# Performance work log

Measured on AMD Instinct MI355X. Metric: run time of the kernel, lower is better.

## Reference

```python
import jax, jax.numpy as jnp
import numpy as np

B, S, T = 16, 128, 128
E, H, D = 512, 512, 1024      # emb, encoder hidden, decoder hidden
VIN, VOUT = 10000, 10000


def setup_inputs() -> dict:
    key = jax.random.key(0)
    ks = iter(jax.random.split(key, 32))
    def w(shape, s=0.02):
        return jax.random.normal(next(ks), shape, jnp.float32) * s
    return {
        "x": jax.random.randint(next(ks), (B, S), 0, VIN),
        "gs_output": jax.random.randint(next(ks), (B, T), 0, VOUT),
        "in_emb": w((VIN, E)),
        "out_emb": w((VOUT, E)),
        "enc_wih0": w((2, 4 * H, E)), "enc_whh0": w((2, 4 * H, H)), "enc_b0": w((2, 4 * H)),
        "enc_wih1": w((2, 4 * H, 2 * H)), "enc_whh1": w((2, 4 * H, H)), "enc_b1": w((2, 4 * H)),
        "dec_wih0": w((4 * D, 2 * H + E)), "dec_whh0": w((4 * D, D)), "dec_b0": w((4 * D,)),
        "dec_wih1": w((4 * D, D)), "dec_whh1": w((4 * D, D)), "dec_b1": w((4 * D,)),
        "attn_w": w((D, 2 * H + D)), "attn_b": w((D,)),
        "attn_v": jax.random.uniform(next(ks), (D,), jnp.float32),
        "out_w": w((VOUT, D)), "out_b": w((VOUT,)),
    }


def _lstm_cell(x, h, c, wih, whh, b):
    # PyTorch gate order: i, f, g, o
    g = x @ wih.T + h @ whh.T + b
    i, f, gg, o = jnp.split(g, 4, axis=-1)
    c = jax.nn.sigmoid(f) * c + jax.nn.sigmoid(i) * jnp.tanh(gg)
    h = jax.nn.sigmoid(o) * jnp.tanh(c)
    return h, c


def _lstm_scan(xs, wih, whh, b, reverse=False):
    # xs: [T, B, in] time-major; returns hidden states [T, B, H]
    Bn, Hh = xs.shape[1], whh.shape[1]
    z = jnp.zeros((Bn, Hh), xs.dtype)
    def step(carry, x):
        h, c = _lstm_cell(x, carry[0], carry[1], wih, whh, b)
        return (h, c), h
    _, hs = jax.lax.scan(step, (z, z), xs, reverse=reverse)
    return hs


def reference(x, gs_output, in_emb, out_emb,
              enc_wih0, enc_whh0, enc_b0, enc_wih1, enc_whh1, enc_b1,
              dec_wih0, dec_whh0, dec_b0, dec_wih1, dec_whh1, dec_b1,
              attn_w, attn_b, attn_v, out_w, out_b):
    # padding_idx=0 rows are zero (matches nn.Embedding(padding_idx=0))
    in_emb = in_emb.at[0].set(0.0)
    out_emb = out_emb.at[0].set(0.0)
    Bn, Sn = x.shape

    # ---- bidirectional 2-layer encoder (eval mode, dropout off) ----
    xs = in_emb[x].transpose(1, 0, 2)  # [S, B, E]
    l0 = jnp.concatenate([
        _lstm_scan(xs, enc_wih0[0], enc_whh0[0], enc_b0[0]),
        _lstm_scan(xs, enc_wih0[1], enc_whh0[1], enc_b0[1], reverse=True)], -1)
    enc = jnp.concatenate([
        _lstm_scan(l0, enc_wih1[0], enc_whh1[0], enc_b1[0]),
        _lstm_scan(l0, enc_wih1[1], enc_whh1[1], enc_b1[1], reverse=True)], -1)
    enc_out = enc.transpose(1, 0, 2)  # [B, S, 2H]

    dec_layers = ((dec_wih0, dec_whh0, dec_b0), (dec_wih1, dec_whh1, dec_b1))

    def dec_step(h, c, inp):
        hs, cs = [], []
        for l, (wih, whh, b) in enumerate(dec_layers):
            nh, nc = _lstm_cell(inp, h[l], c[l], wih, whh, b)
            hs.append(nh); cs.append(nc); inp = nh
        return jnp.stack(hs), jnp.stack(cs), inp

    # torch primes decoder_hidden with one zero-input step from zero state
    h = jnp.zeros((2, Bn, D), jnp.float32)
    c = jnp.zeros((2, Bn, D), jnp.float32)
    h, c, _ = dec_step(h, c, jnp.zeros((Bn, 2 * H + E), jnp.float32))

    gs_emb = out_emb[gs_output].transpose(1, 0, 2)  # [T, B, E]

    def step(carry, emb_t):
        h, c, last_emb = carry
        q = c[-1]  # torch uses decoder_hidden[-1][-1] = last-layer CELL state
        qrep = jnp.broadcast_to(q[:, None, :], (Bn, Sn, D))
        energy = jnp.tanh(jnp.einsum('bsk,dk->bsd', jnp.concatenate([qrep, enc_out], -1), attn_w) + attn_b)
        a = jax.nn.softmax(energy @ attn_v, axis=1)           # [B, S]
        weighted = jnp.einsum('bs,bsh->bh', a, enc_out)       # [B, 2H]
        h2, c2, top = dec_step(h, c, jnp.concatenate([weighted, last_emb], -1))
        logits = top @ out_w.T + out_b                        # [B, Vout]
        return (h2, c2, emb_t), logits

    init = (h, c, jnp.zeros((Bn, E), jnp.float32))
    _, outs = jax.lax.scan(step, init, gs_emb)                # [T, B, Vout]
    return outs.transpose(1, 0, 2)                            # [B, T, Vout]
```

## Files before the change

### kernel.cpp

```cpp
#include <hip/hip_runtime.h>

#define BB 16
#define SS 128
#define TT 128
#define EE 512
#define HH 512
#define DD 1024
#define VO 10000

#define FMA4(A, W, X)              \
  A = fmaf((W).x, (X).x, A);       \
  A = fmaf((W).y, (X).y, A);       \
  A = fmaf((W).z, (X).z, A);       \
  A = fmaf((W).w, (X).w, A)

__device__ __forceinline__ float wred(float s) {
#pragma unroll
  for (int off = 32; off >= 1; off >>= 1) s += __shfl_xor(s, off, 64);
  return s;
}
__device__ __forceinline__ float sigm(float x) { return 1.f / (1.f + expf(-x)); }

__device__ __forceinline__ void stv(float* p, float v) {
  __hip_atomic_store(p, v, __ATOMIC_RELAXED, __HIP_MEMORY_SCOPE_AGENT);
}

__device__ __forceinline__ void gbar2(unsigned* bar, int lb, int nblk, unsigned target) {
  asm volatile("s_waitcnt vmcnt(0) lgkmcnt(0)" ::: "memory");
  __syncthreads();
  if (threadIdx.x == 0)
    __hip_atomic_store(bar + lb * 16, target, __ATOMIC_RELAXED, __HIP_MEMORY_SCOPE_AGENT);
  if (lb == 0) {
    for (int i = threadIdx.x; i < nblk; i += blockDim.x)
      while (__hip_atomic_load(bar + i * 16, __ATOMIC_RELAXED, __HIP_MEMORY_SCOPE_AGENT) <
             target)
        __builtin_amdgcn_s_sleep(1);
    __syncthreads();
    if (threadIdx.x == 0)
      __hip_atomic_store(bar + 8192, target, __ATOMIC_RELAXED, __HIP_MEMORY_SCOPE_AGENT);
  }
  if (threadIdx.x == 0)
    while (__hip_atomic_load(bar + 8192, __ATOMIC_RELAXED, __HIP_MEMORY_SCOPE_AGENT) <
           target)
      __builtin_amdgcn_s_sleep(1);
  __syncthreads();
}

__global__ void gather_k(const int* __restrict__ idx, const float* __restrict__ emb,
                         float* __restrict__ out, int Sn) {
  const int s = blockIdx.x, b = blockIdx.y, tid = threadIdx.x;
  const int id = idx[b * Sn + s];
  float4 v = make_float4(0.f, 0.f, 0.f, 0.f);
  if (id != 0) v = ((const float4*)(emb + (size_t)id * EE))[tid];
  ((float4*)(out + ((size_t)s * BB + b) * EE))[tid] = v;
}

template <int K>
__global__ void gemv16b_k(const float* __restrict__ X, int ldx,
                          const float* __restrict__ W, int ldw,
                          float* __restrict__ G, int M, size_t wz, size_t gz) {
  const int lane = threadIdx.x & 63;
  const int n = blockIdx.x * 4 + (threadIdx.x >> 6);
  const int mg = blockIdx.y;
  const int z = blockIdx.z;
  const float* Xr = X + (size_t)mg * 16 * ldx;
  const float* Wn = W + (size_t)z * wz + (size_t)n * ldw;
  float acc[16];
#pragma unroll
  for (int j = 0; j < 16; ++j) acc[j] = 0.f;
#pragma unroll
  for (int it = 0; it < K / 256; ++it) {
    const int k = it * 256 + lane * 4;
    const float4 w4 = *(const float4*)&Wn[k];
#pragma unroll
    for (int j = 0; j < 16; ++j) {
      const float4 xv = *(const float4*)&Xr[(size_t)j * ldx + k];
      FMA4(acc[j], w4, xv);
    }
  }
#pragma unroll
  for (int j = 0; j < 16; ++j) acc[j] = wred(acc[j]);
  float sel = 0.f;
#pragma unroll
  for (int j = 0; j < 16; ++j)
    if (lane == j) sel = acc[j];
  if (lane < 16) G[(size_t)z * gz + (size_t)n * M + mg * 16 + lane] = sel;
}

__global__ __launch_bounds__(512, 4) void enc_mega7_k(
    const float* __restrict__ gx, const float* __restrict__ whh,
    const float* __restrict__ bias, float* __restrict__ h_all,
    float* __restrict__ seq, int seq_ts, int seq_bs, unsigned* __restrict__ barbase) {
  const int tid = threadIdx.x, lane = tid & 63, lw = tid >> 6;
  const int dir = blockIdx.x >> 7;
  const int lb = blockIdx.x & 127;
  const int w2 = lb * 8 + lw;
  const int d = w2 >> 1, bq = w2 & 1;
  unsigned* bar = barbase + dir * 16384;

  __shared__ float hs[16][512];

  float wr[4][8];
  const float* wsrc = whh + (size_t)dir * (4 * HH * HH);
#pragma unroll
  for (int g = 0; g < 4; ++g)
#pragma unroll
    for (int j = 0; j < 8; ++j)
      wr[g][j] = wsrc[(size_t)(g * HH + d) * HH + j * 64 + lane];
  float bv[4];
#pragma unroll
  for (int g = 0; g < 4; ++g) bv[g] = bias[dir * 4 * HH + g * HH + d];
  const float* gxz = gx + (size_t)dir * ((size_t)4 * HH * 2048);
  float creg = 0.f;
  unsigned bt = 0;

  for (int t = 0; t < SS; ++t) {
    const int idx = dir ? (SS - 1 - t) : t;
    const float* hp = h_all + ((size_t)t * 2 + dir) * (BB * HH);
    for (int i = tid; i < BB * HH / 4; i += 512)
      *(float4*)&((float*)hs)[i * 4] = *(const float4*)&hp[i * 4];
    __syncthreads();
    float acc[4][8];
#pragma unroll
    for (int g = 0; g < 4; ++g)
#pragma unroll
      for (int j = 0; j < 8; ++j) acc[g][j] = 0.f;
#pragma unroll
    for (int kb = 0; kb < 8; ++kb) {
      const int k = kb * 64 + lane;
#pragma unroll
      for (int j = 0; j < 8; ++j) {
        const float xv = hs[bq * 8 + j][k];
#pragma unroll
        for (int g = 0; g < 4; ++g) acc[g][j] = fmaf(wr[g][kb], xv, acc[g][j]);
      }
    }
#pragma unroll
    for (int g = 0; g < 4; ++g)
#pragma unroll
      for (int j = 0; j < 8; ++j) acc[g][j] = wred(acc[g][j]);
    float s0 = 0.f, s1 = 0.f, s2 = 0.f, s3 = 0.f;
#pragma unroll
    for (int j = 0; j < 8; ++j)
      if (lane == j) { s0 = acc[0][j]; s1 = acc[1][j]; s2 = acc[2][j]; s3 = acc[3][j]; }
    if (lane < 8) {
      const int b = bq * 8 + lane;
      const int m = idx * 16 + b;
      const float gi = sigm(s0 + bv[0] + gxz[(size_t)(0 * HH + d) * 2048 + m]);
      const float gf = sigm(s1 + bv[1] + gxz[(size_t)(1 * HH + d) * 2048 + m]);
      const float gg = tanhf(s2 + bv[2] + gxz[(size_t)(2 * HH + d) * 2048 + m]);
      const float go = sigm(s3 + bv[3] + gxz[(size_t)(3 * HH + d) * 2048 + m]);
      const float cn = gf * creg + gi * gg;
      creg = cn;
      const float hv = go * tanhf(cn);
      stv(h_all + ((size_t)(t + 1) * 2 + dir) * (BB * HH) + b * HH + d, hv);
      seq[(size_t)idx * seq_ts + (size_t)b * seq_bs + dir * HH + d] = hv;
    }
    gbar2(bar, lb, 128, ++bt);
  }
}

__global__ __launch_bounds__(1024, 4) void dec_mega7_k(
    const float* __restrict__ gs_emb, const float* __restrict__ encWe,
    const float* __restrict__ enc_out, const float* __restrict__ attn_w,
    const float* __restrict__ attn_b, const float* __restrict__ attn_v,
    const float* __restrict__ wih0, const float* __restrict__ whh0,
    const float* __restrict__ b0, const float* __restrict__ wih1,
    const float* __restrict__ whh1, const float* __restrict__ b1,
    const float* __restrict__ zeros, float* __restrict__ h0_all,
    float* __restrict__ h1_all, float* __restrict__ c1_all, float* __restrict__ wtd_all,
    float* __restrict__ qW_all, float* __restrict__ scores_all,
    unsigned* __restrict__ bar) {
  const int tid = threadIdx.x, lane = tid & 63, lw = tid >> 6;
  const int blk = blockIdx.x;
  const int w = blk * 16 + lw;
  const int d = w >> 2, bq = w & 3;
  const int b_att = blk >> 4, shard = blk & 15;

  __shared__ float sco[SS];
  __shared__ float sred[16][64];

  const float* w0i0 = wih0 + (size_t)(0 * DD + d) * 1536;
  const float* w0i1 = wih0 + (size_t)(1 * DD + d) * 1536;
  const float* w0i2 = wih0 + (size_t)(2 * DD + d) * 1536;
  const float* w0i3 = wih0 + (size_t)(3 * DD + d) * 1536;
  const float* w0h0 = whh0 + (size_t)(0 * DD + d) * 1024;
  const float* w0h1 = whh0 + (size_t)(1 * DD + d) * 1024;
  const float* w0h2 = whh0 + (size_t)(2 * DD + d) * 1024;
  const float* w0h3 = whh0 + (size_t)(3 * DD + d) * 1024;
  const float* w1i0 = wih1 + (size_t)(0 * DD + d) * 1024;
  const float* w1i1 = wih1 + (size_t)(1 * DD + d) * 1024;
  const float* w1i2 = wih1 + (size_t)(2 * DD + d) * 1024;
  const float* w1i3 = wih1 + (size_t)(3 * DD + d) * 1024;
  const float* w1h0 = whh1 + (size_t)(0 * DD + d) * 1024;
  const float* w1h1 = whh1 + (size_t)(1 * DD + d) * 1024;
  const float* w1h2 = whh1 + (size_t)(2 * DD + d) * 1024;
  const float* w1h3 = whh1 + (size_t)(3 * DD + d) * 1024;
  float bv0[4], bv1[4];
#pragma unroll
  for (int g = 0; g < 4; ++g) { bv0[g] = b0[g * DD + d]; bv1[g] = b1[g * DD + d]; }
  const float abv = attn_b[d];
  float c0 = 0.f, c1 = 0.f;
  unsigned bt = 0;

  if (lane < 4) {
    const float cn = sigm(bv0[0]) * tanhf(bv0[2]);
    c0 = cn;
    stv(h0_all + (bq * 4 + lane) * DD + d, sigm(bv0[3]) * tanhf(cn));
  }
  gbar2(bar, blk, 256, ++bt);
  {
    float acc[4][4];
#pragma unroll
    for (int g = 0; g < 4; ++g)
#pragma unroll
      for (int j = 0; j < 4; ++j) acc[g][j] = 0.f;
#pragma unroll
    for (int it = 0; it < 4; ++it) {
      const int k = it * 256 + lane * 4;
      const float4 q0 = *(const float4*)&w1i0[k];
      const float4 q1 = *(const float4*)&w1i1[k];
      const float4 q2 = *(const float4*)&w1i2[k];
      const float4 q3 = *(const float4*)&w1i3[k];
#pragma unroll
      for (int j = 0; j < 4; ++j) {
        const float4 xv = *(const float4*)&h0_all[(bq * 4 + j) * DD + k];
        FMA4(acc[0][j], q0, xv);
        FMA4(acc[1][j], q1, xv);
        FMA4(acc[2][j], q2, xv);
        FMA4(acc[3][j], q3, xv);
      }
    }
#pragma unroll
    for (int g = 0; g < 4; ++g)
#pragma unroll
      for (int j = 0; j < 4; ++j) acc[g][j] = wred(acc[g][j]);
    float s[4] = {0.f, 0.f, 0.f, 0.f};
#pragma unroll
    for (int j = 0; j < 4; ++j)
      if (lane == j) { s[0] = acc[0][j]; s[1] = acc[1][j]; s[2] = acc[2][j]; s[3] = acc[3][j]; }
    if (lane < 4) {
      const int b = bq * 4 + lane;
      const float cn = sigm(s[0] + bv1[0]) * tanhf(s[2] + bv1[2]);
      c1 = cn;
      stv(c1_all + b * DD + d, cn);
      stv(h1_all + b * DD + d, sigm(s[3] + bv1[3]) * tanhf(cn));
    }
  }
  gbar2(bar, blk, 256, ++bt);

  for (int t = 0; t < TT; ++t) {
    {
      const float* cb = c1_all + (size_t)t * (BB * DD);
      const float* wq = attn_w + (size_t)d * 2048;
      float qa[4] = {0.f, 0.f, 0.f, 0.f};
#pragma unroll
      for (int it = 0; it < 4; ++it) {
        const int k = it * 256 + lane * 4;
        const float4 w4 = *(const float4*)&wq[k];
#pragma unroll
        for (int j = 0; j < 4; ++j) {
          const float4 xv = *(const float4*)&cb[(bq * 4 + j) * DD + k];
          FMA4(qa[j], w4, xv);
        }
      }
#pragma unroll
      for (int j = 0; j < 4; ++j) qa[j] = wred(qa[j]);
      float sel = 0.f;
#pragma unroll
      for (int j = 0; j < 4; ++j)
        if (lane == j) sel = qa[j];
      if (lane < 4)
        stv(qW_all + (size_t)t * (BB * DD) + (bq * 4 + lane) * DD + d, sel + abv);
    }
    gbar2(bar, blk, 256, ++bt);
    if (lw < 8) {
      const int s = shard * 8 + lw;
      const float* ew = encWe + ((size_t)(b_att * SS + s)) * DD;
      const float* qb = qW_all + (size_t)t * (BB * DD) + b_att * DD;
      float a = 0.f;
#pragma unroll
      for (int it = 0; it < 4; ++it) {
        const int k = it * 256 + lane * 4;
        const float4 e4 = *(const float4*)&ew[k];
        const float4 q4 = *(const float4*)&qb[k];
        const float4 v4 = *(const float4*)&attn_v[k];
        a += v4.x * tanhf(q4.x + e4.x) + v4.y * tanhf(q4.y + e4.y) +
             v4.z * tanhf(q4.z + e4.z) + v4.w * tanhf(q4.w + e4.w);
      }
      a = wred(a);
      if (lane == 0) stv(scores_all + (size_t)t * (BB * SS) + b_att * SS + s, a);
    }
    gbar2(bar, blk, 256, ++bt);
    {
      if (tid < SS) sco[tid] = scores_all[(size_t)t * (BB * SS) + b_att * SS + tid];
      __syncthreads();
      float m = -1e30f;
      for (int s = 0; s < SS; ++s) m = fmaxf(m, sco[s]);
      __syncthreads();
      if (tid < SS) sco[tid] = expf(sco[tid] - m);
      __syncthreads();
      float sum = 0.f;
      for (int s = 0; s < SS; ++s) sum += sco[s];
      const float inv = 1.f / sum;
      float p = 0.f;
#pragma unroll
      for (int i = 0; i < 8; ++i) {
        const int s = lw * 8 + i;
        p += sco[s] * enc_out[((size_t)(b_att * SS + s)) * DD + shard * 64 + lane];
      }
      sred[lw][lane] = p;
      __syncthreads();
      if (lw == 0) {
        float a2 = 0.f;
#pragma unroll
        for (int i = 0; i < 16; ++i) a2 += sred[i][lane];
        stv(wtd_all + (size_t)t * (BB * DD) + b_att * DD + shard * 64 + lane, a2 * inv);
      }
    }
    gbar2(bar, blk, 256, ++bt);
    {
      const float* xw = wtd_all + (size_t)t * (BB * DD);
      const float* em = t ? gs_emb + (size_t)(t - 1) * (BB * EE) : zeros;
      const float* hp = h0_all + (size_t)t * (BB * DD);
      float acc[4][4];
#pragma unroll
      for (int g = 0; g < 4; ++g)
#pragma unroll
        for (int j = 0; j < 4; ++j) acc[g][j] = 0.f;
#pragma unroll
      for (int it = 0; it < 4; ++it) {
        const int k = it * 256 + lane * 4;
        const float4 q0 = *(const float4*)&w0i0[k];
        const float4 q1 = *(const float4*)&w0i1[k];
        const float4 q2 = *(const float4*)&w0i2[k];
        const float4 q3 = *(const float4*)&w0i3[k];
#pragma unroll
        for (int j = 0; j < 4; ++j) {
          const float4 xv = *(const float4*)&xw[(bq * 4 + j) * DD + k];
          FMA4(acc[0][j], q0, xv);
          FMA4(acc[1][j], q1, xv);
          FMA4(acc[2][j], q2, xv);
          FMA4(acc[3][j], q3, xv);
        }
      }
#pragma unroll
      for (int it = 4; it < 6; ++it) {
        const int k = it * 256 + lane * 4;
        const float4 q0 = *(const float4*)&w0i0[k];
        const float4 q1 = *(const float4*)&w0i1[k];
        const float4 q2 = *(const float4*)&w0i2[k];
        const float4 q3 = *(const float4*)&w0i3[k];
#pragma unroll
        for (int j = 0; j < 4; ++j) {
          const float4 xv = *(const float4*)&em[(bq * 4 + j) * EE + (k - 1024)];
          FMA4(acc[0][j], q0, xv);
          FMA4(acc[1][j], q1, xv);
          FMA4(acc[2][j], q2, xv);
          FMA4(acc[3][j], q3, xv);
        }
      }
#pragma unroll
      for (int it = 0; it < 4; ++it) {
        const int k = it * 256 + lane * 4;
        const float4 q0 = *(const float4*)&w0h0[k];
        const float4 q1 = *(const float4*)&w0h1[k];
        const float4 q2 = *(const float4*)&w0h2[k];
        const float4 q3 = *(const float4*)&w0h3[k];
#pragma unroll
        for (int j = 0; j < 4; ++j) {
          const float4 xv = *(const float4*)&hp[(bq * 4 + j) * DD + k];
          FMA4(acc[0][j], q0, xv);
          FMA4(acc[1][j], q1, xv);
          FMA4(acc[2][j], q2, xv);
          FMA4(acc[3][j], q3, xv);
        }
      }
#pragma unroll
      for (int g = 0; g < 4; ++g)
#pragma unroll
        for (int j = 0; j < 4; ++j) acc[g][j] = wred(acc[g][j]);
      float s[4] = {0.f, 0.f, 0.f, 0.f};
#pragma unroll
      for (int j = 0; j < 4; ++j)
        if (lane == j) { s[0] = acc[0][j]; s[1] = acc[1][j]; s[2] = acc[2][j]; s[3] = acc[3][j]; }
      if (lane < 4) {
        const int b = bq * 4 + lane;
        const float cn = sigm(s[1] + bv0[1]) * c0 + sigm(s[0] + bv0[0]) * tanhf(s[2] + bv0[2]);
        c0 = cn;
        stv(h0_all + (size_t)(t + 1) * (BB * DD) + b * DD + d,
            sigm(s[3] + bv0[3]) * tanhf(cn));
      }
    }
    gbar2(bar, blk, 256, ++bt);
    {
      const float* h0 = h0_all + (size_t)(t + 1) * (BB * DD);
      const float* h1p = h1_all + (size_t)t * (BB * DD);
      float acc[4][4];
#pragma unroll
      for (int g = 0; g < 4; ++g)
#pragma unroll
        for (int j = 0; j < 4; ++j) acc[g][j] = 0.f;
#pragma unroll
      for (int it = 0; it < 4; ++it) {
        const int k = it * 256 + lane * 4;
        const float4 q0 = *(const float4*)&w1i0[k];
        const float4 q1 = *(const float4*)&w1i1[k];
        const float4 q2 = *(const float4*)&w1i2[k];
        const float4 q3 = *(const float4*)&w1i3[k];
#pragma unroll
        for (int j = 0; j < 4; ++j) {
          const float4 xv = *(const float4*)&h0[(bq * 4 + j) * DD + k];
          FMA4(acc[0][j], q0, xv);
          FMA4(acc[1][j], q1, xv);
          FMA4(acc[2][j], q2, xv);
          FMA4(acc[3][j], q3, xv);
        }
      }
#pragma unroll
      for (int it = 0; it < 4; ++it) {
        const int k = it * 256 + lane * 4;
        const float4 q0 = *(const float4*)&w1h0[k];
        const float4 q1 = *(const float4*)&w1h1[k];
        const float4 q2 = *(const float4*)&w1h2[k];
        const float4 q3 = *(const float4*)&w1h3[k];
#pragma unroll
        for (int j = 0; j < 4; ++j) {
          const float4 xv = *(const float4*)&h1p[(bq * 4 + j) * DD + k];
          FMA4(acc[0][j], q0, xv);
          FMA4(acc[1][j], q1, xv);
          FMA4(acc[2][j], q2, xv);
          FMA4(acc[3][j], q3, xv);
        }
      }
#pragma unroll
      for (int g = 0; g < 4; ++g)
#pragma unroll
        for (int j = 0; j < 4; ++j) acc[g][j] = wred(acc[g][j]);
      float s[4] = {0.f, 0.f, 0.f, 0.f};
#pragma unroll
      for (int j = 0; j < 4; ++j)
        if (lane == j) { s[0] = acc[0][j]; s[1] = acc[1][j]; s[2] = acc[2][j]; s[3] = acc[3][j]; }
      if (lane < 4) {
        const int b = bq * 4 + lane;
        const float cn = sigm(s[1] + bv1[1]) * c1 + sigm(s[0] + bv1[0]) * tanhf(s[2] + bv1[2]);
        c1 = cn;
        stv(c1_all + (size_t)(t + 1) * (BB * DD) + b * DD + d, cn);
        stv(h1_all + (size_t)(t + 1) * (BB * DD) + b * DD + d,
            sigm(s[3] + bv1[3]) * tanhf(cn));
      }
    }
    gbar2(bar, blk, 256, ++bt);
  }
}

__global__ __launch_bounds__(512) void encwe2_k(const float* __restrict__ enc_out,
                                                const float* __restrict__ attn_w,
                                                float* __restrict__ encWe) {
  const int tid = threadIdx.x, lane = tid & 63, lw = tid >> 6;
  const int mg = blockIdx.x;
  const int nq = blockIdx.y;
  __shared__ float xsl[16][1024];
  for (int i = tid; i < 16 * 1024 / 4; i += 512)
    *(float4*)&((float*)xsl)[i * 4] =
        *(const float4*)&enc_out[(size_t)mg * 16 * 1024 + i * 4];
  __syncthreads();
#pragma unroll 1
  for (int nn = 0; nn < 8; ++nn) {
    const int n = nq * 64 + lw * 8 + nn;
    float acc[16];
#pragma unroll
    for (int j = 0; j < 16; ++j) acc[j] = 0.f;
#pragma unroll
    for (int it = 0; it < 4; ++it) {
      const int k = it * 256 + lane * 4;
      const float4 w4 = *(const float4*)&attn_w[(size_t)n * 2048 + 1024 + k];
#pragma unroll
      for (int j = 0; j < 16; ++j) {
        const float4 xv = *(const float4*)&xsl[j][k];
        FMA4(acc[j], w4, xv);
      }
    }
#pragma unroll
    for (int j = 0; j < 16; ++j) acc[j] = wred(acc[j]);
    float sel = 0.f;
#pragma unroll
    for (int j = 0; j < 16; ++j)
      if (lane == j) sel = acc[j];
    if (lane < 16) encWe[((size_t)mg * 16 + lane) * 1024 + n] = sel;
  }
}

__global__ __launch_bounds__(1024, 4) void logits2_k(const float* __restrict__ h1all,
                                                     const float* __restrict__ out_w,
                                                     const float* __restrict__ out_b,
                                                     float* __restrict__ out) {
  const int tid = threadIdx.x, lane = tid & 63, lw = tid >> 6;
  const int t = blockIdx.x;
  const int oq = blockIdx.y;
  __shared__ float hs[16][1024];
  const float* h1 = h1all + (size_t)t * (BB * DD);
  for (int i = tid; i < BB * DD / 4; i += 1024)
    *(float4*)&((float*)hs)[i * 4] = *(const float4*)&h1[i * 4];
  __syncthreads();
  const int obase = oq * 80 + lw * 5;
#pragma unroll
  for (int p = 0; p < 3; ++p) {
    const int nr = (p < 2) ? 2 : 1;
    const int o0 = obase + p * 2;
    float accA[16], accB[16];
#pragma unroll
    for (int b = 0; b < 16; ++b) { accA[b] = 0.f; accB[b] = 0.f; }
    const float* wr0 = out_w + (size_t)o0 * DD;
    const float* wr1 = wr0 + DD;
#pragma unroll
    for (int it = 0; it < 4; ++it) {
      const int k = it * 256 + lane * 4;
      const float4 wa = *(const float4*)&wr0[k];
      float4 wb = make_float4(0.f, 0.f, 0.f, 0.f);
      if (nr == 2) wb = *(const float4*)&wr1[k];
#pragma unroll
      for (int b = 0; b < 16; ++b) {
        const float4 xv = *(const float4*)&hs[b][k];
        FMA4(accA[b], wa, xv);
        if (nr == 2) { FMA4(accB[b], wb, xv); }
      }
    }
#pragma unroll
    for (int b = 0; b < 16; ++b) {
      accA[b] = wred(accA[b]);
      if (nr == 2) accB[b] = wred(accB[b]);
    }
    float sA = 0.f, sB = 0.f;
#pragma unroll
    for (int b = 0; b < 16; ++b)
      if (lane == b) { sA = accA[b]; sB = accB[b]; }
    if (lane < 16) {
      out[(size_t)lane * TT * VO + (size_t)t * VO + o0] = sA + out_b[o0];
      if (nr == 2) out[(size_t)lane * TT * VO + (size_t)t * VO + o0 + 1] = sB + out_b[o0 + 1];
    }
  }
}

extern "C" void kernel_launch(void* const* d_in, const int* in_sizes, int n_in,
                              void* d_out, int out_size, void* d_ws, size_t ws_size,
                              hipStream_t stream) {
  const int* x = (const int*)d_in[0];
  const int* gs = (const int*)d_in[1];
  const float* in_emb = (const float*)d_in[2];
  const float* out_emb = (const float*)d_in[3];
  const float* ewih0 = (const float*)d_in[4];
  const float* ewhh0 = (const float*)d_in[5];
  const float* eb0 = (const float*)d_in[6];
  const float* ewih1 = (const float*)d_in[7];
  const float* ewhh1 = (const float*)d_in[8];
  const float* eb1 = (const float*)d_in[9];
  const float* dwih0 = (const float*)d_in[10];
  const float* dwhh0 = (const float*)d_in[11];
  const float* db0 = (const float*)d_in[12];
  const float* dwih1 = (const float*)d_in[13];
  const float* dwhh1 = (const float*)d_in[14];
  const float* db1 = (const float*)d_in[15];
  const float* attn_w = (const float*)d_in[16];
  const float* attn_b = (const float*)d_in[17];
  const float* attn_v = (const float*)d_in[18];
  const float* out_w = (const float*)d_in[19];
  const float* out_b = (const float*)d_in[20];
  float* out = (float*)d_out;

  float* ws = (float*)d_ws;
  size_t off = 0;
  auto alloc = [&](size_t n) { float* p = ws + off; off += n; return p; };
  unsigned* bar = (unsigned*)alloc(5 * 16384);
  float* zeros = alloc(BB * DD);
  float* ehA = alloc((size_t)(SS + 1) * 2 * BB * HH);
  float* ehB = alloc(2 * BB * HH);
  const size_t state_n = off;
  alloc((size_t)SS * 2 * BB * HH);
  float* h0_all = alloc((size_t)(TT + 1) * BB * DD);
  float* h1_all = alloc((size_t)(TT + 1) * BB * DD);
  float* c1_all = alloc((size_t)(TT + 1) * BB * DD);
  float* wtd_all = alloc((size_t)TT * BB * DD);
  float* qW_all = alloc((size_t)TT * BB * DD);
  float* scores_all = alloc((size_t)TT * BB * SS);
  float* xs_emb = alloc((size_t)SS * BB * EE);
  float* gs_emb = alloc((size_t)TT * BB * EE);
  float* l0 = alloc((size_t)SS * BB * (2 * HH));
  float* enc_out = alloc((size_t)BB * SS * (2 * HH));
  float* encWe = alloc((size_t)BB * SS * DD);
  float* gxA = alloc(2ull * 2048ull * 2048ull);
  (void)ws_size; (void)in_sizes; (void)n_in; (void)out_size;

  hipMemsetAsync(d_ws, 0, state_n * sizeof(float), stream);

  gather_k<<<dim3(SS, BB), 128, 0, stream>>>(x, in_emb, xs_emb, SS);
  gather_k<<<dim3(TT, BB), 128, 0, stream>>>(gs, out_emb, gs_emb, TT);

  gemv16b_k<EE><<<dim3(512, 128, 2), 256, 0, stream>>>(
      xs_emb, EE, ewih0, EE, gxA, 2048, (size_t)4 * HH * EE, 2048ull * 2048ull);
  enc_mega7_k<<<256, 512, 0, stream>>>(gxA, ewhh0, eb0, ehA, l0, BB * 2 * HH, 2 * HH, bar);
  gemv16b_k<2 * HH><<<dim3(512, 128, 2), 256, 0, stream>>>(
      l0, 2 * HH, ewih1, 2 * HH, gxA, 2048, (size_t)4 * HH * 2 * HH, 2048ull * 2048ull);
  enc_mega7_k<<<256, 512, 0, stream>>>(gxA, ewhh1, eb1, ehB, enc_out, 2 * HH, SS * 2 * HH,
                                       bar + 2 * 16384);
  encwe2_k<<<dim3(128, 16), 512, 0, stream>>>(enc_out, attn_w, encWe);

  dec_mega7_k<<<256, 1024, 0, stream>>>(gs_emb, encWe, enc_out, attn_w, attn_b, attn_v,
                                        dwih0, dwhh0, db0, dwih1, dwhh1, db1, zeros,
                                        h0_all, h1_all, c1_all, wtd_all, qW_all,
                                        scores_all, bar + 4 * 16384);

  logits2_k<<<dim3(TT, 125), 1024, 0, stream>>>(h1_all + BB * DD, out_w, out_b, out);
}
```

Baseline: 16.86 ms.

## Remap decoder mega-kernel so each wave owns one gate across all batches

```diff
diff --git a/kernel.cpp b/kernel.cpp
--- a/kernel.cpp
+++ b/kernel.cpp
@@ -160,7 +160,7 @@
   }
 }
 
-__global__ __launch_bounds__(1024, 4) void dec_mega7_k(
+__global__ __launch_bounds__(1024, 4) void dec_mega8_k(
     const float* __restrict__ gs_emb, const float* __restrict__ encWe,
     const float* __restrict__ enc_out, const float* __restrict__ attn_w,
     const float* __restrict__ attn_b, const float* __restrict__ attn_v,
@@ -173,78 +173,61 @@
     unsigned* __restrict__ bar) {
   const int tid = threadIdx.x, lane = tid & 63, lw = tid >> 6;
   const int blk = blockIdx.x;
-  const int w = blk * 16 + lw;
-  const int d = w >> 2, bq = w & 3;
+  const int g = lw & 3;
+  const int dloc = lw >> 2;
+  const int d = blk * 4 + dloc;
   const int b_att = blk >> 4, shard = blk & 15;
 
+  __shared__ float xch[4][4][16];
   __shared__ float sco[SS];
   __shared__ float sred[16][64];
 
-  const float* w0i0 = wih0 + (size_t)(0 * DD + d) * 1536;
-  const float* w0i1 = wih0 + (size_t)(1 * DD + d) * 1536;
-  const float* w0i2 = wih0 + (size_t)(2 * DD + d) * 1536;
-  const float* w0i3 = wih0 + (size_t)(3 * DD + d) * 1536;
-  const float* w0h0 = whh0 + (size_t)(0 * DD + d) * 1024;
-  const float* w0h1 = whh0 + (size_t)(1 * DD + d) * 1024;
-  const float* w0h2 = whh0 + (size_t)(2 * DD + d) * 1024;
-  const float* w0h3 = whh0 + (size_t)(3 * DD + d) * 1024;
-  const float* w1i0 = wih1 + (size_t)(0 * DD + d) * 1024;
-  const float* w1i1 = wih1 + (size_t)(1 * DD + d) * 1024;
-  const float* w1i2 = wih1 + (size_t)(2 * DD + d) * 1024;
-  const float* w1i3 = wih1 + (size_t)(3 * DD + d) * 1024;
-  const float* w1h0 = whh1 + (size_t)(0 * DD + d) * 1024;
-  const float* w1h1 = whh1 + (size_t)(1 * DD + d) * 1024;
-  const float* w1h2 = whh1 + (size_t)(2 * DD + d) * 1024;
-  const float* w1h3 = whh1 + (size_t)(3 * DD + d) * 1024;
+  const float* w0i = wih0 + (size_t)(g * DD + d) * 1536;
+  const float* w0h = whh0 + (size_t)(g * DD + d) * 1024;
+  const float* w1i = wih1 + (size_t)(g * DD + d) * 1024;
+  const float* w1h = whh1 + (size_t)(g * DD + d) * 1024;
   float bv0[4], bv1[4];
 #pragma unroll
-  for (int g = 0; g < 4; ++g) { bv0[g] = b0[g * DD + d]; bv1[g] = b1[g * DD + d]; }
+  for (int gg = 0; gg < 4; ++gg) { bv0[gg] = b0[gg * DD + d]; bv1[gg] = b1[gg * DD + d]; }
   const float abv = attn_b[d];
   float c0 = 0.f, c1 = 0.f;
   unsigned bt = 0;
 
-  if (lane < 4) {
+  if (g == 0 && lane < 16) {
     const float cn = sigm(bv0[0]) * tanhf(bv0[2]);
     c0 = cn;
-    stv(h0_all + (bq * 4 + lane) * DD + d, sigm(bv0[3]) * tanhf(cn));
+    stv(h0_all + lane * DD + d, sigm(bv0[3]) * tanhf(cn));
   }
   gbar2(bar, blk, 256, ++bt);
   {
-    float acc[4][4];
-#pragma unroll
-    for (int g = 0; g < 4; ++g)
-#pragma unroll
-      for (int j = 0; j < 4; ++j) acc[g][j] = 0.f;
+    float4 wv[4];
+#pragma unroll
+    for (int it = 0; it < 4; ++it) wv[it] = *(const float4*)&w1i[it * 256 + lane * 4];
+    float acc[16];
+#pragma unroll
+    for (int b = 0; b < 16; ++b) acc[b] = 0.f;
 #pragma unroll
     for (int it = 0; it < 4; ++it) {
       const int k = it * 256 + lane * 4;
-      const float4 q0 = *(const float4*)&w1i0[k];
-      const float4 q1 = *(const float4*)&w1i1[k];
-      const float4 q2 = *(const float4*)&w1i2[k];
-      const float4 q3 = *(const float4*)&w1i3[k];
-#pragma unroll
-      for (int j = 0; j < 4; ++j) {
-        const float4 xv = *(const float4*)&h0_all[(bq * 4 + j) * DD + k];
-        FMA4(acc[0][j], q0, xv);
-        FMA4(acc[1][j], q1, xv);
-        FMA4(acc[2][j], q2, xv);
-        FMA4(acc[3][j], q3, xv);
-      }
-    }
-#pragma unroll
-    for (int g = 0; g < 4; ++g)
-#pragma unroll
-      for (int j = 0; j < 4; ++j) acc[g][j] = wred(acc[g][j]);
-    float s[4] = {0.f, 0.f, 0.f, 0.f};
-#pragma unroll
-    for (int j = 0; j < 4; ++j)
-      if (lane == j) { s[0] = acc[0][j]; s[1] = acc[1][j]; s[2] = acc[2][j]; s[3] = acc[3][j]; }
-    if (lane < 4) {
-      const int b = bq * 4 + lane;
-      const float cn = sigm(s[0] + bv1[0]) * tanhf(s[2] + bv1[2]);
+#pragma unroll
+      for (int b = 0; b < 16; ++b) {
+        const float4 xv = *(const float4*)&h0_all[b * DD + k];
+        FMA4(acc[b], wv[it], xv);
+      }
+    }
+#pragma unroll
+    for (int b = 0; b < 16; ++b) acc[b] = wred(acc[b]);
+    float sel = 0.f;
+#pragma unroll
+    for (int b = 0; b < 16; ++b)
+      if (lane == b) sel = acc[b];
+    if (lane < 16) xch[dloc][g][lane] = sel;
+    __syncthreads();
+    if (g == 0 && lane < 16) {
+      const float cn = sigm(xch[dloc][0][lane] + bv1[0]) * tanhf(xch[dloc][2][lane] + bv1[2]);
       c1 = cn;
-      stv(c1_all + b * DD + d, cn);
-      stv(h1_all + b * DD + d, sigm(s[3] + bv1[3]) * tanhf(cn));
+      stv(c1_all + lane * DD + d, cn);
+      stv(h1_all + lane * DD + d, sigm(xch[dloc][3][lane] + bv1[3]) * tanhf(cn));
     }
   }
   gbar2(bar, blk, 256, ++bt);
@@ -252,26 +235,30 @@
   for (int t = 0; t < TT; ++t) {
     {
       const float* cb = c1_all + (size_t)t * (BB * DD);
-      const float* wq = attn_w + (size_t)d * 2048;
-      float qa[4] = {0.f, 0.f, 0.f, 0.f};
-#pragma unroll
-      for (int it = 0; it < 4; ++it) {
-        const int k = it * 256 + lane * 4;
-        const float4 w4 = *(const float4*)&wq[k];
-#pragma unroll
-        for (int j = 0; j < 4; ++j) {
-          const float4 xv = *(const float4*)&cb[(bq * 4 + j) * DD + k];
-          FMA4(qa[j], w4, xv);
-        }
-      }
-#pragma unroll
-      for (int j = 0; j < 4; ++j) qa[j] = wred(qa[j]);
+      const int k = g * 256 + lane * 4;
+      const float4 w4 = *(const float4*)&attn_w[(size_t)d * 2048 + k];
+      float acc[16];
+#pragma unroll
+      for (int b = 0; b < 16; ++b) acc[b] = 0.f;
+#pragma unroll
+      for (int b = 0; b < 16; ++b) {
+        const float4 xv = *(const float4*)&cb[b * DD + k];
+        FMA4(acc[b], w4, xv);
+      }
+#pragma unroll
+      for (int b = 0; b < 16; ++b) acc[b] = wred(acc[b]);
       float sel = 0.f;
 #pragma unroll
-      for (int j = 0; j < 4; ++j)
-        if (lane == j) sel = qa[j];
-      if (lane < 4)
-        stv(qW_all + (size_t)t * (BB * DD) + (bq * 4 + lane) * DD + d, sel + abv);
+      for (int b = 0; b < 16; ++b)
+        if (lane == b) sel = acc[b];
+      if (lane < 16) xch[dloc][g][lane] = sel;
+      __syncthreads();
+      if (g == 0 && lane < 16) {
+        const float q = xch[dloc][0][lane] + xch[dloc][1][lane] + xch[dloc][2][lane] +
+                        xch[dloc][3][lane] + abv;
+        stv(qW_all + (size_t)t * (BB * DD) + lane * DD + d, q);
+      }
+      __syncthreads();
     }
     gbar2(bar, blk, 256, ++bt);
     if (lw < 8) {
@@ -323,132 +310,111 @@
       const float* xw = wtd_all + (size_t)t * (BB * DD);
       const float* em = t ? gs_emb + (size_t)(t - 1) * (BB * EE) : zeros;
       const float* hp = h0_all + (size_t)t * (BB * DD);
-      float acc[4][4];
-#pragma unroll
-      for (int g = 0; g < 4; ++g)
-#pragma unroll
-        for (int j = 0; j < 4; ++j) acc[g][j] = 0.f;
+      float4 wv[10];
+#pragma unroll
+      for (int it = 0; it < 6; ++it) wv[it] = *(const float4*)&w0i[it * 256 + lane * 4];
+#pragma unroll
+      for (int it = 6; it < 10; ++it)
+        wv[it] = *(const float4*)&w0h[(it - 6) * 256 + lane * 4];
+      float acc[16];
+#pragma unroll
+      for (int b = 0; b < 16; ++b) acc[b] = 0.f;
 #pragma unroll
       for (int it = 0; it < 4; ++it) {
         const int k = it * 256 + lane * 4;
-        const float4 q0 = *(const float4*)&w0i0[k];
-        const float4 q1 = *(const float4*)&w0i1[k];
-        const float4 q2 = *(const float4*)&w0i2[k];
-        const float4 q3 = *(const float4*)&w0i3[k];
-#pragma unroll
-        for (int j = 0; j < 4; ++j) {
-          const float4 xv = *(const float4*)&xw[(bq * 4 + j) * DD + k];
-          FMA4(acc[0][j], q0, xv);
-          FMA4(acc[1][j], q1, xv);
-          FMA4(acc[2][j], q2, xv);
-          FMA4(acc[3][j], q3, xv);
+#pragma unroll
+        for (int b = 0; b < 16; ++b) {
+          const float4 xv = *(const float4*)&xw[b * DD + k];
+          FMA4(acc[b], wv[it], xv);
         }
       }
 #pragma unroll
       for (int it = 4; it < 6; ++it) {
-        const int k = it * 256 + lane * 4;
-        const float4 q0 = *(const float4*)&w0i0[k];
-        const float4 q1 = *(const float4*)&w0i1[k];
-        const float4 q2 = *(const float4*)&w0i2[k];
-        const float4 q3 = *(const float4*)&w0i3[k];
-#pragma unroll
-        for (int j = 0; j < 4; ++j) {
-          const float4 xv = *(const float4*)&em[(bq * 4 + j) * EE + (k - 1024)];
-          FMA4(acc[0][j], q0, xv);
-          FMA4(acc[1][j], q1, xv);
-          FMA4(acc[2][j], q2, xv);
-          FMA4(acc[3][j], q3, xv);
+        const int k = (it - 4) * 256 + lane * 4;
+#pragma unroll
+        for (int b = 0; b < 16; ++b) {
+          const float4 xv = *(const float4*)&em[b * EE + k];
+          FMA4(acc[b], wv[it], xv);
         }
       }
 #pragma unroll
-      for (int it = 0; it < 4; ++it) {
-        const int k = it * 256 + lane * 4;
-        const float4 q0 = *(const float4*)&w0h0[k];
-        const float4 q1 = *(const float4*)&w0h1[k];
-        const float4 q2 = *(const float4*)&w0h2[k];
-        const float4 q3 = *(const float4*)&w0h3[k];
-#pragma unroll
-        for (int j = 0; j < 4; ++j) {
-          const float4 xv = *(const float4*)&hp[(bq * 4 + j) * DD + k];
-          FMA4(acc[0][j], q0, xv);
-          FMA4(acc[1][j], q1, xv);
-          FMA4(acc[2][j], q2, xv);
-          FMA4(acc[3][j], q3, xv);
+      for (int it = 6; it < 10; ++it) {
+        const int k = (it - 6) * 256 + lane * 4;
+#pragma unroll
+        for (int b = 0; b < 16; ++b) {
+          const float4 xv = *(const float4*)&hp[b * DD + k];
+          FMA4(acc[b], wv[it], xv);
         }
       }
 #pragma unroll
-      for (int g = 0; g < 4; ++g)
-#pragma unroll
-        for (int j = 0; j < 4; ++j) acc[g][j] = wred(acc[g][j]);
-      float s[4] = {0.f, 0.f, 0.f, 0.f};
-#pragma unroll
-      for (int j = 0; j < 4; ++j)
-        if (lane == j) { s[0] = acc[0][j]; s[1] = acc[1][j]; s[2] = acc[2][j]; s[3] = acc[3][j]; }
-      if (lane < 4) {
-        const int b = bq * 4 + lane;
-        const float cn = sigm(s[1] + bv0[1]) * c0 + sigm(s[0] + bv0[0]) * tanhf(s[2] + bv0[2]);
+      for (int b = 0; b < 16; ++b) acc[b] = wred(acc[b]);
+      float sel = 0.f;
+#pragma unroll
+      for (int b = 0; b < 16; ++b)
+        if (lane == b) sel = acc[b];
+      if (lane < 16) xch[dloc][g][lane] = sel;
+      __syncthreads();
+      if (g == 0 && lane < 16) {
+        const float gi = sigm(xch[dloc][0][lane] + bv0[0]);
+        const float gf = sigm(xch[dloc][1][lane] + bv0[1]);
+        const float gg = tanhf(xch[dloc][2][lane] + bv0[2]);
+        const float go = sigm(xch[dloc][3][lane] + bv0[3]);
+        const float cn = gf * c0 + gi * gg;
         c0 = cn;
-        stv(h0_all + (size_t)(t + 1) * (BB * DD) + b * DD + d,
-            sigm(s[3] + bv0[3]) * tanhf(cn));
-      }
+        stv(h0_all + (size_t)(t + 1) * (BB * DD) + lane * DD + d, go * tanhf(cn));
+      }
+      __syncthreads();
     }
     gbar2(bar, blk, 256, ++bt);
     {
       const float* h0 = h0_all + (size_t)(t + 1) * (BB * DD);
       const float* h1p = h1_all + (size_t)t * (BB * DD);
-      float acc[4][4];
-#pragma unroll
-      for (int g = 0; g < 4; ++g)
-#pragma unroll
-        for (int j = 0; j < 4; ++j) acc[g][j] = 0.f;
+      float4 wv[8];
+#pragma unroll
+      for (int it = 0; it < 4; ++it) wv[it] = *(const float4*)&w1i[it * 256 + lane * 4];
+#pragma unroll
+      for (int it = 4; it < 8; ++it)
+        wv[it] = *(const float4*)&w1h[(it - 4) * 256 + lane * 4];
+      float acc[16];
+#pragma unroll
+      for (int b = 0; b < 16; ++b) acc[b] = 0.f;
 #pragma unroll
       for (int it = 0; it < 4; ++it) {
         const int k = it * 256 + lane * 4;
-        const float4 q0 = *(const float4*)&w1i0[k];
-        const float4 q1 = *(const float4*)&w1i1[k];
-        const float4 q2 = *(const float4*)&w1i2[k];
-        const float4 q3 = *(const float4*)&w1i3[k];
-#pragma unroll
-        for (int j = 0; j < 4; ++j) {
-          const float4 xv = *(const float4*)&h0[(bq * 4 + j) * DD + k];
-          FMA4(acc[0][j], q0, xv);
-          FMA4(acc[1][j], q1, xv);
-          FMA4(acc[2][j], q2, xv);
-          FMA4(acc[3][j], q3, xv);
+#pragma unroll
+        for (int b = 0; b < 16; ++b) {
+          const float4 xv = *(const float4*)&h0[b * DD + k];
+          FMA4(acc[b], wv[it], xv);
         }
       }
 #pragma unroll
-      for (int it = 0; it < 4; ++it) {
-        const int k = it * 256 + lane * 4;
-        const float4 q0 = *(const float4*)&w1h0[k];
-        const float4 q1 = *(const float4*)&w1h1[k];
-        const float4 q2 = *(const float4*)&w1h2[k];
-        const float4 q3 = *(const float4*)&w1h3[k];
-#pragma unroll
-        for (int j = 0; j < 4; ++j) {
-          const float4 xv = *(const float4*)&h1p[(bq * 4 + j) * DD + k];
-          FMA4(acc[0][j], q0, xv);
-          FMA4(acc[1][j], q1, xv);
-          FMA4(acc[2][j], q2, xv);
-          FMA4(acc[3][j], q3, xv);
+      for (int it = 4; it < 8; ++it) {
+        const int k = (it - 4) * 256 + lane * 4;
+#pragma unroll
+        for (int b = 0; b < 16; ++b) {
+          const float4 xv = *(const float4*)&h1p[b * DD + k];
+          FMA4(acc[b], wv[it], xv);
         }
       }
 #pragma unroll
-      for (int g = 0; g < 4; ++g)
-#pragma unroll
-        for (int j = 0; j < 4; ++j) acc[g][j] = wred(acc[g][j]);
-      float s[4] = {0.f, 0.f, 0.f, 0.f};
-#pragma unroll
-      for (int j = 0; j < 4; ++j)
-        if (lane == j) { s[0] = acc[0][j]; s[1] = acc[1][j]; s[2] = acc[2][j]; s[3] = acc[3][j]; }
-      if (lane < 4) {
-        const int b = bq * 4 + lane;
-        const float cn = sigm(s[1] + bv1[1]) * c1 + sigm(s[0] + bv1[0]) * tanhf(s[2] + bv1[2]);
+      for (int b = 0; b < 16; ++b) acc[b] = wred(acc[b]);
+      float sel = 0.f;
+#pragma unroll
+      for (int b = 0; b < 16; ++b)
+        if (lane == b) sel = acc[b];
+      if (lane < 16) xch[dloc][g][lane] = sel;
+      __syncthreads();
+      if (g == 0 && lane < 16) {
+        const float gi = sigm(xch[dloc][0][lane] + bv1[0]);
+        const float gf = sigm(xch[dloc][1][lane] + bv1[1]);
+        const float gg = tanhf(xch[dloc][2][lane] + bv1[2]);
+        const float go = sigm(xch[dloc][3][lane] + bv1[3]);
+        const float cn = gf * c1 + gi * gg;
         c1 = cn;
-        stv(c1_all + (size_t)(t + 1) * (BB * DD) + b * DD + d, cn);
-        stv(h1_all + (size_t)(t + 1) * (BB * DD) + b * DD + d,
-            sigm(s[3] + bv1[3]) * tanhf(cn));
-      }
+        stv(c1_all + (size_t)(t + 1) * (BB * DD) + lane * DD + d, cn);
+        stv(h1_all + (size_t)(t + 1) * (BB * DD) + lane * DD + d, go * tanhf(cn));
+      }
+      __syncthreads();
     }
     gbar2(bar, blk, 256, ++bt);
   }
@@ -605,7 +571,7 @@
                                        bar + 2 * 16384);
   encwe2_k<<<dim3(128, 16), 512, 0, stream>>>(enc_out, attn_w, encWe);
 
-  dec_mega7_k<<<256, 1024, 0, stream>>>(gs_emb, encWe, enc_out, attn_w, attn_b, attn_v,
+  dec_mega8_k<<<256, 1024, 0, stream>>>(gs_emb, encWe, enc_out, attn_w, attn_b, attn_v,
                                         dwih0, dwhh0, db0, dwih1, dwhh1, db1, zeros,
                                         h0_all, h1_all, c1_all, wtd_all, qW_all,
                                         scores_all, bar + 4 * 16384);
```

New measurement: 21.00 ms. 1.25x slower.
